# Optimization experiments

Hardware: AMD Instinct MI355X
Metric: run time of the kernel (lower is better)

Reference implementation:

```python
import jax, jax.numpy as jnp
import numpy as np

D_MODEL = 768
N_HEADS = 12
D_K = D_MODEL // N_HEADS
NEG = -1e9


def setup_inputs() -> dict:
    key = jax.random.key(0)
    ks = jax.random.split(key, 10)
    B, S = 2, 2048
    x = jax.random.normal(ks[0], (B, S, D_MODEL), dtype=jnp.float32)
    # causal mask, broadcastable over batch and heads
    mask = jnp.tril(jnp.ones((S, S), dtype=jnp.int32))[None, None]
    scale = 1.0 / np.sqrt(D_MODEL)
    def lin(k):
        return jax.random.normal(k, (D_MODEL, D_MODEL), dtype=jnp.float32) * scale
    return {
        "x": x, "mask": mask,
        "wq": lin(ks[1]), "bq": jnp.zeros((D_MODEL,), jnp.float32),
        "wk": lin(ks[2]), "bk": jnp.zeros((D_MODEL,), jnp.float32),
        "wv": lin(ks[3]), "bv": jnp.zeros((D_MODEL,), jnp.float32),
        "wo": lin(ks[4]), "bo": jnp.zeros((D_MODEL,), jnp.float32),
    }


def reference(x, mask, wq, bq, wk, bk, wv, bv, wo, bo):
    B, S, _ = x.shape
    def split_heads(t):  # [B,S,D] -> [B,H,S,dk]
        return t.reshape(B, S, N_HEADS, D_K).transpose(0, 2, 1, 3)
    q = split_heads(x @ wq + bq)
    k = split_heads(x @ wk + bk)
    v = split_heads(x @ wv + bv)
    scores = jnp.einsum("bhqd,bhkd->bhqk", q, k) / jnp.sqrt(jnp.float32(D_K))
    scores = jnp.where(mask == 0, NEG, scores)
    attn = jax.nn.softmax(scores, axis=-1)
    # dropout is identity in eval mode
    ctx = jnp.einsum("bhqk,bhkd->bhqd", attn, v)
    ctx = ctx.transpose(0, 2, 1, 3).reshape(B, S, D_MODEL)
    return ctx @ wo + bo
```

## Files before the change

kernel.cpp:

```cpp
#include <hip/hip_runtime.h>
#include <hip/hip_bf16.h>
#include <stdint.h>

#define DM   768
#define NH   12
#define DKH  64
#define BB   2
#define SS   2048
#define MT   (BB*SS)
#define NQKV (3*DM)

typedef __attribute__((ext_vector_type(8))) short short8;
typedef __attribute__((ext_vector_type(4))) float f32x4;

__device__ __forceinline__ unsigned short f2bf(float f) {
    union { float f; unsigned u; } v; v.f = f;
    unsigned r = v.u + 0x7fffu + ((v.u >> 16) & 1u);
    return (unsigned short)(r >> 16);
}

__device__ __forceinline__ void gload_lds16(const unsigned short* g, unsigned short* l) {
    __builtin_amdgcn_global_load_lds((const __attribute__((address_space(1))) void*)g,
                                     (__attribute__((address_space(3))) void*)l, 16, 0, 0);
}

__launch_bounds__(256)
__global__ void k_conv(const float* __restrict__ x, unsigned short* __restrict__ xb,
                       const float* __restrict__ wq, const float* __restrict__ wk,
                       const float* __restrict__ wv, const float* __restrict__ wo,
                       unsigned short* __restrict__ wT) {
    __shared__ float tile[32][33];
    const int t = threadIdx.x;
    if (blockIdx.x < 3072) {
        int i = blockIdx.x * 256 + t;
        const float4 v = ((const float4*)x)[i];
        ushort4 o;
        o.x = f2bf(v.x); o.y = f2bf(v.y); o.z = f2bf(v.z); o.w = f2bf(v.w);
        ((ushort4*)xb)[i] = o;
    } else {
        const int cid = blockIdx.x - 3072;
        const int sel = cid / 576;
        const int rem = cid - sel * 576;
        const int kb = rem / 24, nb = rem - (rem / 24) * 24;
        const float* w = (sel == 0) ? wq : (sel == 1) ? wk : (sel == 2) ? wv : wo;
        const int k0 = kb * 32, n0 = nb * 32;
        const int tx = t & 31, ty = t >> 5;
        #pragma unroll
        for (int j = 0; j < 4; j++)
            tile[ty + 8*j][tx] = w[(size_t)(k0 + ty + 8*j) * DM + n0 + tx];
        __syncthreads();
        #pragma unroll
        for (int j = 0; j < 4; j++)
            wT[(size_t)(sel*DM + n0 + ty + 8*j) * DM + k0 + tx] = f2bf(tile[tx][ty + 8*j]);
    }
}

__launch_bounds__(256)
__global__ void k_gemm_qkv(const unsigned short* __restrict__ xb,
                           const unsigned short* __restrict__ wT,
                           const float* __restrict__ bq, const float* __restrict__ bk,
                           const float* __restrict__ bv,
                           unsigned short* __restrict__ Qb,
                           unsigned short* __restrict__ Kb,
                           unsigned short* __restrict__ Vt) {
    __shared__ __align__(16) unsigned short As[128][32];
    __shared__ __align__(16) unsigned short Bs[128][32];
    const int t = threadIdx.x;
    const int m0 = blockIdx.x * 128;
    const int n0 = blockIdx.y * 128;
    const int wid = t >> 6, lane = t & 63, q4 = lane >> 4, l16 = lane & 15;
    const int wm = (wid >> 1) * 64, wn = (wid & 1) * 64;

    const int srow = wid * 32 + (lane >> 2);
    const int koff = (lane & 3) * 8;
    const unsigned short* AgL = xb + (size_t)(m0 + srow) * DM + koff;
    const unsigned short* AgH = AgL + (size_t)16 * DM;
    const unsigned short* BgL = wT + (size_t)(n0 + srow) * DM + koff;
    const unsigned short* BgH = BgL + (size_t)16 * DM;
    unsigned short* ldsA1 = &As[wid*32][0];
    unsigned short* ldsA2 = &As[wid*32 + 16][0];
    unsigned short* ldsB1 = &Bs[wid*32][0];
    unsigned short* ldsB2 = &Bs[wid*32 + 16][0];

    f32x4 acc[4][4];
    for (int i = 0; i < 4; i++) for (int j = 0; j < 4; j++)
        acc[i][j] = (f32x4){0.f, 0.f, 0.f, 0.f};

    for (int kt = 0; kt < DM; kt += 32) {
        gload_lds16(AgL + kt, ldsA1);
        gload_lds16(AgH + kt, ldsA2);
        gload_lds16(BgL + kt, ldsB1);
        gload_lds16(BgH + kt, ldsB2);
        __syncthreads();
        short8 af[4], bf[4];
        for (int i = 0; i < 4; i++) af[i] = *(const short8*)&As[wm + i*16 + l16][q4*8];
        for (int i = 0; i < 4; i++) bf[i] = *(const short8*)&Bs[wn + i*16 + l16][q4*8];
        for (int mi = 0; mi < 4; mi++)
            for (int ni = 0; ni < 4; ni++)
                acc[mi][ni] = __builtin_amdgcn_mfma_f32_16x16x32_bf16(af[mi], bf[ni], acc[mi][ni], 0, 0, 0);
        __syncthreads();
    }

    const int sel = n0 / DM;
    const float* bias = (sel == 0) ? bq : (sel == 1) ? bk : bv;
    for (int ni = 0; ni < 4; ni++) {
        const int col = n0 + wn + ni*16 + l16;
        const int c = col - sel * DM;
        const float bsv = bias[c];
        const int h = c >> 6, d = c & 63;
        for (int mi = 0; mi < 4; mi++) {
            for (int r = 0; r < 4; r++) {
                const int row = m0 + wm + mi*16 + q4*4 + r;
                const int b = row >> 11, s = row & 2047;
                const int bh = b * NH + h;
                float v = acc[mi][ni][r] + bsv;
                if (sel == 0) {
                    Qb[(bh*SS + s)*DKH + d] = f2bf(v * 0.125f);
                } else if (sel == 1) {
                    Kb[(bh*SS + s)*DKH + d] = f2bf(v);
                } else {
                    Vt[(bh*DKH + d)*SS + s] = f2bf(v);
                }
            }
        }
    }
}

__launch_bounds__(256)
__global__ void k_attn(const unsigned short* __restrict__ Qb,
                       const unsigned short* __restrict__ Kb,
                       const unsigned short* __restrict__ Vt,
                       unsigned short* __restrict__ ctx) {
    __shared__ __align__(16) unsigned short Ks[2][64][72];
    __shared__ __align__(16) unsigned short Vs[2][64][72];
    __shared__ __align__(16) unsigned short P[4][16][68];
    const int t = threadIdx.x;
    const int wid = t >> 6, lane = t & 63, q4 = lane >> 4, l16 = lane & 15;
    const int lin = blockIdx.x;
    const int bh = lin % (BB * NH);
    const int qblk = 31 - lin / (BB * NH);
    const int b = bh / NH, h = bh - b * NH;
    const int qw = qblk * 64 + wid * 16;

    const unsigned short* Qp = Qb + (size_t)bh * SS * DKH;
    const unsigned short* Kp = Kb + (size_t)bh * SS * DKH;
    const unsigned short* Vp = Vt + (size_t)bh * DKH * SS;

    const int sr = t >> 3;
    const int sc = (t & 7) * 8;

    short8 qf[2];
    for (int kc = 0; kc < 2; kc++)
        qf[kc] = *(const short8*)(Qp + (qw + l16)*DKH + kc*32 + q4*8);

    f32x4 accO[4];
    for (int j = 0; j < 4; j++) accO[j] = (f32x4){0.f, 0.f, 0.f, 0.f};
    float lacc[4] = {0.f, 0.f, 0.f, 0.f};

    {
        uint4 k0 = *(const uint4*)(Kp + (size_t)(sr)      * DKH + sc);
        uint4 k1 = *(const uint4*)(Kp + (size_t)(sr + 32) * DKH + sc);
        uint4 v0 = *(const uint4*)(Vp + (size_t)(sr)      * SS  + sc);
        uint4 v1 = *(const uint4*)(Vp + (size_t)(sr + 32) * SS  + sc);
        *(uint4*)&Ks[0][sr][sc]      = k0;
        *(uint4*)&Ks[0][sr + 32][sc] = k1;
        *(uint4*)&Vs[0][sr][sc]      = v0;
        *(uint4*)&Vs[0][sr + 32][sc] = v1;
    }
    __syncthreads();

    for (int kt = 0; kt <= qblk; kt++) {
        const int cb = kt & 1, nb = cb ^ 1;
        const bool hasN = (kt < qblk);
        uint4 nk0, nk1, nv0, nv1;
        if (hasN) {
            const int kn = (kt + 1) * 64;
            nk0 = *(const uint4*)(Kp + (size_t)(kn + sr)      * DKH + sc);
            nk1 = *(const uint4*)(Kp + (size_t)(kn + sr + 32) * DKH + sc);
            nv0 = *(const uint4*)(Vp + (size_t)(sr)      * SS + kn + sc);
            nv1 = *(const uint4*)(Vp + (size_t)(sr + 32) * SS + kn + sc);
        }
        short8 kf[4][2];
        #pragma unroll
        for (int ni = 0; ni < 4; ni++)
            #pragma unroll
            for (int kc = 0; kc < 2; kc++)
                kf[ni][kc] = *(const short8*)&Ks[cb][ni*16 + l16][kc*32 + q4*8];
        f32x4 S[4];
        #pragma unroll
        for (int j = 0; j < 4; j++) S[j] = (f32x4){0.f, 0.f, 0.f, 0.f};
        #pragma unroll
        for (int ni = 0; ni < 4; ni++) {
            S[ni] = __builtin_amdgcn_mfma_f32_16x16x32_bf16(qf[0], kf[ni][0], S[ni], 0, 0, 0);
            S[ni] = __builtin_amdgcn_mfma_f32_16x16x32_bf16(qf[1], kf[ni][1], S[ni], 0, 0, 0);
        }
        short8 vf[4][2];
        #pragma unroll
        for (int ndi = 0; ndi < 4; ndi++)
            #pragma unroll
            for (int kc = 0; kc < 2; kc++)
                vf[ndi][kc] = *(const short8*)&Vs[cb][ndi*16 + l16][kc*32 + q4*8];
        if (kt == qblk) {
            #pragma unroll
            for (int ni = 0; ni < 4; ni++) {
                const int pr = q4*4, pc = ni*16 + l16;
                if (ni > wid) {
                    P[wid][pr+0][pc] = 0; P[wid][pr+1][pc] = 0;
                    P[wid][pr+2][pc] = 0; P[wid][pr+3][pc] = 0;
                    continue;
                }
                float p[4];
                if (ni == wid) {
                    #pragma unroll
                    for (int r = 0; r < 4; r++) {
                        const int qrow = qw + q4*4 + r;
                        const int key = qblk*64 + ni*16 + l16;
                        p[r] = (key > qrow) ? 0.f : __expf(S[ni][r]);
                        lacc[r] += p[r];
                    }
                } else {
                    #pragma unroll
                    for (int r = 0; r < 4; r++) { p[r] = __expf(S[ni][r]); lacc[r] += p[r]; }
                }
                union { __hip_bfloat162 v; unsigned u; } u01, u23;
                u01.v = __float22bfloat162_rn(make_float2(p[0], p[1]));
                u23.v = __float22bfloat162_rn(make_float2(p[2], p[3]));
                P[wid][pr+0][pc] = (unsigned short)(u01.u & 0xffffu);
                P[wid][pr+1][pc] = (unsigned short)(u01.u >> 16);
                P[wid][pr+2][pc] = (unsigned short)(u23.u & 0xffffu);
                P[wid][pr+3][pc] = (unsigned short)(u23.u >> 16);
            }
        } else {
            #pragma unroll
            for (int ni = 0; ni < 4; ni++) {
                float p[4];
                #pragma unroll
                for (int r = 0; r < 4; r++) { p[r] = __expf(S[ni][r]); lacc[r] += p[r]; }
                union { __hip_bfloat162 v; unsigned u; } u01, u23;
                u01.v = __float22bfloat162_rn(make_float2(p[0], p[1]));
                u23.v = __float22bfloat162_rn(make_float2(p[2], p[3]));
                const int pr = q4*4, pc = ni*16 + l16;
                P[wid][pr+0][pc] = (unsigned short)(u01.u & 0xffffu);
                P[wid][pr+1][pc] = (unsigned short)(u01.u >> 16);
                P[wid][pr+2][pc] = (unsigned short)(u23.u & 0xffffu);
                P[wid][pr+3][pc] = (unsigned short)(u23.u >> 16);
            }
        }
        asm volatile("s_waitcnt lgkmcnt(0)" ::: "memory");
        short8 pf[2];
        #pragma unroll
        for (int kc = 0; kc < 2; kc++)
            pf[kc] = *(const short8*)&P[wid][l16][kc*32 + q4*8];
        #pragma unroll
        for (int ndi = 0; ndi < 4; ndi++)
            #pragma unroll
            for (int kc = 0; kc < 2; kc++)
                accO[ndi] = __builtin_amdgcn_mfma_f32_16x16x32_bf16(pf[kc], vf[ndi][kc], accO[ndi], 0, 0, 0);
        if (hasN) {
            *(uint4*)&Ks[nb][sr][sc]      = nk0;
            *(uint4*)&Ks[nb][sr + 32][sc] = nk1;
            *(uint4*)&Vs[nb][sr][sc]      = nv0;
            *(uint4*)&Vs[nb][sr + 32][sc] = nv1;
        }
        __syncthreads();
    }

    for (int r = 0; r < 4; r++) {
        float l = lacc[r];
        for (int off = 1; off < 16; off <<= 1) l += __shfl_xor(l, off);
        const float inv = 1.0f / l;
        const int s = qw + q4*4 + r;
        for (int ni = 0; ni < 4; ni++)
            ctx[((size_t)(b*SS + s))*DM + h*64 + ni*16 + l16] = f2bf(accO[ni][r] * inv);
    }
}

__launch_bounds__(256)
__global__ void k_gemm_proj(const unsigned short* __restrict__ ctx,
                            const unsigned short* __restrict__ woT,
                            const float* __restrict__ bo,
                            float* __restrict__ out) {
    __shared__ __align__(16) unsigned short As[128][32];
    __shared__ __align__(16) unsigned short Bs[64][32];
    const int t = threadIdx.x;
    const int m0 = blockIdx.x * 128;
    const int n0 = blockIdx.y * 64;
    const int wid = t >> 6, lane = t & 63, q4 = lane >> 4, l16 = lane & 15;
    const int wm = (wid >> 1) * 64, wn = (wid & 1) * 32;

    const int srowA = wid * 32 + (lane >> 2);
    const int srowB = wid * 16 + (lane >> 2);
    const int koff = (lane & 3) * 8;
    const unsigned short* AgL = ctx + (size_t)(m0 + srowA) * DM + koff;
    const unsigned short* AgH = AgL + (size_t)16 * DM;
    const unsigned short* BgL = woT + (size_t)(n0 + srowB) * DM + koff;
    unsigned short* ldsA1 = &As[wid*32][0];
    unsigned short* ldsA2 = &As[wid*32 + 16][0];
    unsigned short* ldsB1 = &Bs[wid*16][0];

    f32x4 acc[4][2];
    for (int i = 0; i < 4; i++) for (int j = 0; j < 2; j++)
        acc[i][j] = (f32x4){0.f, 0.f, 0.f, 0.f};

    for (int kt = 0; kt < DM; kt += 32) {
        gload_lds16(AgL + kt, ldsA1);
        gload_lds16(AgH + kt, ldsA2);
        gload_lds16(BgL + kt, ldsB1);
        __syncthreads();
        short8 af[4], bf[2];
        for (int i = 0; i < 4; i++) af[i] = *(const short8*)&As[wm + i*16 + l16][q4*8];
        for (int i = 0; i < 2; i++) bf[i] = *(const short8*)&Bs[wn + i*16 + l16][q4*8];
        for (int mi = 0; mi < 4; mi++)
            for (int ni = 0; ni < 2; ni++)
                acc[mi][ni] = __builtin_amdgcn_mfma_f32_16x16x32_bf16(af[mi], bf[ni], acc[mi][ni], 0, 0, 0);
        __syncthreads();
    }

    for (int ni = 0; ni < 2; ni++) {
        const int col = n0 + wn + ni*16 + l16;
        const float bsv = bo[col];
        for (int mi = 0; mi < 4; mi++) {
            for (int r = 0; r < 4; r++) {
                const int row = m0 + wm + mi*16 + q4*4 + r;
                out[(size_t)row * DM + col] = acc[mi][ni][r] + bsv;
            }
        }
    }
}

extern "C" void kernel_launch(void* const* d_in, const int* in_sizes, int n_in,
                              void* d_out, int out_size, void* d_ws, size_t ws_size,
                              hipStream_t stream) {
    const float* x  = (const float*)d_in[0];
    const float* wq = (const float*)d_in[2];
    const float* bq = (const float*)d_in[3];
    const float* wk = (const float*)d_in[4];
    const float* bk = (const float*)d_in[5];
    const float* wv = (const float*)d_in[6];
    const float* bv = (const float*)d_in[7];
    const float* wo = (const float*)d_in[8];
    const float* bo = (const float*)d_in[9];
    float* out = (float*)d_out;

    unsigned short* xb  = (unsigned short*)d_ws;
    unsigned short* wT  = xb + (size_t)MT * DM;
    unsigned short* Qb  = wT + (size_t)4 * DM * DM;
    unsigned short* Kb  = Qb + (size_t)BB * NH * SS * DKH;
    unsigned short* Vt  = Kb + (size_t)BB * NH * SS * DKH;
    unsigned short* ctx = Vt + (size_t)BB * NH * SS * DKH;

    k_conv<<<3072 + 2304, 256, 0, stream>>>(x, xb, wq, wk, wv, wo, wT);
    dim3 g1(MT / 128, NQKV / 128);
    k_gemm_qkv<<<g1, 256, 0, stream>>>(xb, wT, bq, bk, bv, Qb, Kb, Vt);
    k_attn<<<dim3(32 * BB * NH), 256, 0, stream>>>(Qb, Kb, Vt, ctx);
    dim3 g3(MT / 128, DM / 64);
    k_gemm_proj<<<g3, 256, 0, stream>>>(ctx, wT + (size_t)3 * DM * DM, bo, out);
}
```

Measured before the change: 176.2 us.

## Restructure attention kernel: 128-row query tiles, swizzled LDS, transposed MFMA, custom block order

The attention kernel now processes 128 query rows per block, 32 per wave, so each K/V tile loaded into LDS is reused by twice as many queries. It also swaps to an XOR-swizzled unpadded LDS layout and computes S^T and O^T through swapped MFMA operands, which allows packed P stores and vectorized ctx writes. A remapped block ordering balances the causal workload, waves skip fully masked tiles, and s_setprio plus a 3-blocks-per-CU launch bound are added. The grid shrinks to 384 blocks, which may reduce occupancy, and the higher register count per wave is a risk.

Measured after the change: 185.0 us. +5.0%, slower.

```diff
diff --git a/kernel.cpp b/kernel.cpp
--- a/kernel.cpp
+++ b/kernel.cpp
@@ -126,152 +126,173 @@
     }
 }
 
-__launch_bounds__(256)
+__launch_bounds__(256, 3)
 __global__ void k_attn(const unsigned short* __restrict__ Qb,
                        const unsigned short* __restrict__ Kb,
                        const unsigned short* __restrict__ Vt,
                        unsigned short* __restrict__ ctx) {
-    __shared__ __align__(16) unsigned short Ks[2][64][72];
-    __shared__ __align__(16) unsigned short Vs[2][64][72];
-    __shared__ __align__(16) unsigned short P[4][16][68];
+    __shared__ __align__(16) unsigned short Ks[2][64*64];
+    __shared__ __align__(16) unsigned short Vs[2][64*64];
+    __shared__ __align__(16) unsigned short P2[4][32*64];
     const int t = threadIdx.x;
     const int wid = t >> 6, lane = t & 63, q4 = lane >> 4, l16 = lane & 15;
+
     const int lin = blockIdx.x;
-    const int bh = lin % (BB * NH);
-    const int qblk = 31 - lin / (BB * NH);
+    int g;
+    if (lin < 128)      g = 128 + lin;
+    else if (lin < 256) g = lin - 128;
+    else                g = 639 - lin;
+    const int bh  = g % 24;
+    const int qsb = 15 - g / 24;
+    const int KT  = 2*qsb + 1;
     const int b = bh / NH, h = bh - b * NH;
-    const int qw = qblk * 64 + wid * 16;
+    const int qw = qsb*128 + wid*32;
+    const int ktw = (qw + 31) >> 6;
 
     const unsigned short* Qp = Qb + (size_t)bh * SS * DKH;
     const unsigned short* Kp = Kb + (size_t)bh * SS * DKH;
     const unsigned short* Vp = Vt + (size_t)bh * DKH * SS;
 
-    const int sr = t >> 3;
-    const int sc = (t & 7) * 8;
-
-    short8 qf[2];
-    for (int kc = 0; kc < 2; kc++)
-        qf[kc] = *(const short8*)(Qp + (qw + l16)*DKH + kc*32 + q4*8);
-
-    f32x4 accO[4];
-    for (int j = 0; j < 4; j++) accO[j] = (f32x4){0.f, 0.f, 0.f, 0.f};
-    float lacc[4] = {0.f, 0.f, 0.f, 0.f};
+    const int sr  = t >> 3;
+    const int sc8 = (t & 7) * 8;
+    const int scs = sc8 ^ ((sr & 7) * 8);
+    const int swz = (l16 & 7) * 8;
+
+    short8 qf[2][2];
+    #pragma unroll
+    for (int c = 0; c < 2; c++)
+        #pragma unroll
+        for (int kc = 0; kc < 2; kc++)
+            qf[c][kc] = *(const short8*)(Qp + (size_t)(qw + c*16 + l16)*DKH + kc*32 + q4*8);
+
+    f32x4 accO[2][4];
+    #pragma unroll
+    for (int c = 0; c < 2; c++)
+        #pragma unroll
+        for (int j = 0; j < 4; j++) accO[c][j] = (f32x4){0.f, 0.f, 0.f, 0.f};
+    float lacc[2] = {0.f, 0.f};
 
     {
-        uint4 k0 = *(const uint4*)(Kp + (size_t)(sr)      * DKH + sc);
-        uint4 k1 = *(const uint4*)(Kp + (size_t)(sr + 32) * DKH + sc);
-        uint4 v0 = *(const uint4*)(Vp + (size_t)(sr)      * SS  + sc);
-        uint4 v1 = *(const uint4*)(Vp + (size_t)(sr + 32) * SS  + sc);
-        *(uint4*)&Ks[0][sr][sc]      = k0;
-        *(uint4*)&Ks[0][sr + 32][sc] = k1;
-        *(uint4*)&Vs[0][sr][sc]      = v0;
-        *(uint4*)&Vs[0][sr + 32][sc] = v1;
+        *(uint4*)&Ks[0][ sr      *64 + scs] = *(const uint4*)(Kp + (size_t) sr      *DKH + sc8);
+        *(uint4*)&Ks[0][(sr+32)*64 + scs]   = *(const uint4*)(Kp + (size_t)(sr+32)  *DKH + sc8);
+        *(uint4*)&Vs[0][ sr      *64 + scs] = *(const uint4*)(Vp + (size_t) sr      *SS  + sc8);
+        *(uint4*)&Vs[0][(sr+32)*64 + scs]   = *(const uint4*)(Vp + (size_t)(sr+32)  *SS  + sc8);
     }
     __syncthreads();
 
-    for (int kt = 0; kt <= qblk; kt++) {
+    for (int kt = 0; kt <= KT; kt++) {
         const int cb = kt & 1, nb = cb ^ 1;
-        const bool hasN = (kt < qblk);
+        const bool hasN = (kt < KT);
         uint4 nk0, nk1, nv0, nv1;
         if (hasN) {
             const int kn = (kt + 1) * 64;
-            nk0 = *(const uint4*)(Kp + (size_t)(kn + sr)      * DKH + sc);
-            nk1 = *(const uint4*)(Kp + (size_t)(kn + sr + 32) * DKH + sc);
-            nv0 = *(const uint4*)(Vp + (size_t)(sr)      * SS + kn + sc);
-            nv1 = *(const uint4*)(Vp + (size_t)(sr + 32) * SS + kn + sc);
-        }
-        short8 kf[4][2];
-        #pragma unroll
-        for (int ni = 0; ni < 4; ni++)
+            nk0 = *(const uint4*)(Kp + (size_t)(kn + sr)      * DKH + sc8);
+            nk1 = *(const uint4*)(Kp + (size_t)(kn + sr + 32) * DKH + sc8);
+            nv0 = *(const uint4*)(Vp + (size_t)(sr)      * SS + kn + sc8);
+            nv1 = *(const uint4*)(Vp + (size_t)(sr + 32) * SS + kn + sc8);
+        }
+        if (kt <= ktw) {
+            f32x4 St[2][4];
             #pragma unroll
-            for (int kc = 0; kc < 2; kc++)
-                kf[ni][kc] = *(const short8*)&Ks[cb][ni*16 + l16][kc*32 + q4*8];
-        f32x4 S[4];
-        #pragma unroll
-        for (int j = 0; j < 4; j++) S[j] = (f32x4){0.f, 0.f, 0.f, 0.f};
-        #pragma unroll
-        for (int ni = 0; ni < 4; ni++) {
-            S[ni] = __builtin_amdgcn_mfma_f32_16x16x32_bf16(qf[0], kf[ni][0], S[ni], 0, 0, 0);
-            S[ni] = __builtin_amdgcn_mfma_f32_16x16x32_bf16(qf[1], kf[ni][1], S[ni], 0, 0, 0);
-        }
-        short8 vf[4][2];
-        #pragma unroll
-        for (int ndi = 0; ndi < 4; ndi++)
-            #pragma unroll
-            for (int kc = 0; kc < 2; kc++)
-                vf[ndi][kc] = *(const short8*)&Vs[cb][ndi*16 + l16][kc*32 + q4*8];
-        if (kt == qblk) {
+            for (int c = 0; c < 2; c++)
+                #pragma unroll
+                for (int ni = 0; ni < 4; ni++) St[c][ni] = (f32x4){0.f, 0.f, 0.f, 0.f};
+            __builtin_amdgcn_s_setprio(1);
             #pragma unroll
             for (int ni = 0; ni < 4; ni++) {
-                const int pr = q4*4, pc = ni*16 + l16;
-                if (ni > wid) {
-                    P[wid][pr+0][pc] = 0; P[wid][pr+1][pc] = 0;
-                    P[wid][pr+2][pc] = 0; P[wid][pr+3][pc] = 0;
-                    continue;
+                const int rbase = (ni*16 + l16) * 64;
+                short8 kf0 = *(const short8*)&Ks[cb][rbase + ((     q4*8) ^ swz)];
+                short8 kf1 = *(const short8*)&Ks[cb][rbase + ((32 + q4*8) ^ swz)];
+                St[0][ni] = __builtin_amdgcn_mfma_f32_16x16x32_bf16(kf0, qf[0][0], St[0][ni], 0, 0, 0);
+                St[0][ni] = __builtin_amdgcn_mfma_f32_16x16x32_bf16(kf1, qf[0][1], St[0][ni], 0, 0, 0);
+                St[1][ni] = __builtin_amdgcn_mfma_f32_16x16x32_bf16(kf0, qf[1][0], St[1][ni], 0, 0, 0);
+                St[1][ni] = __builtin_amdgcn_mfma_f32_16x16x32_bf16(kf1, qf[1][1], St[1][ni], 0, 0, 0);
+            }
+            __builtin_amdgcn_s_setprio(0);
+            if (kt < ktw) {
+                #pragma unroll
+                for (int c = 0; c < 2; c++) {
+                    const int prow = (c*16 + l16) * 64;
+                    #pragma unroll
+                    for (int ni = 0; ni < 4; ni++) {
+                        float p0 = __expf(St[c][ni][0]), p1 = __expf(St[c][ni][1]);
+                        float p2 = __expf(St[c][ni][2]), p3 = __expf(St[c][ni][3]);
+                        lacc[c] += (p0 + p1) + (p2 + p3);
+                        union { __hip_bfloat162 v; unsigned u; } u01, u23;
+                        u01.v = __float22bfloat162_rn(make_float2(p0, p1));
+                        u23.v = __float22bfloat162_rn(make_float2(p2, p3));
+                        uint2 pk; pk.x = u01.u; pk.y = u23.u;
+                        *(uint2*)&P2[wid][prow + ((ni*16 + q4*4) ^ swz)] = pk;
+                    }
                 }
-                float p[4];
-                if (ni == wid) {
+            } else {
+                const int kb0 = kt * 64;
+                #pragma unroll
+                for (int c = 0; c < 2; c++) {
+                    const int qrow = qw + c*16 + l16;
+                    const int prow = (c*16 + l16) * 64;
                     #pragma unroll
-                    for (int r = 0; r < 4; r++) {
-                        const int qrow = qw + q4*4 + r;
-                        const int key = qblk*64 + ni*16 + l16;
-                        p[r] = (key > qrow) ? 0.f : __expf(S[ni][r]);
-                        lacc[r] += p[r];
+                    for (int ni = 0; ni < 4; ni++) {
+                        const int key0 = kb0 + ni*16 + q4*4;
+                        float p[4];
+                        #pragma unroll
+                        for (int r = 0; r < 4; r++) {
+                            p[r] = (key0 + r > qrow) ? 0.f : __expf(St[c][ni][r]);
+                            lacc[c] += p[r];
+                        }
+                        union { __hip_bfloat162 v; unsigned u; } u01, u23;
+                        u01.v = __float22bfloat162_rn(make_float2(p[0], p[1]));
+                        u23.v = __float22bfloat162_rn(make_float2(p[2], p[3]));
+                        uint2 pk; pk.x = u01.u; pk.y = u23.u;
+                        *(uint2*)&P2[wid][prow + ((ni*16 + q4*4) ^ swz)] = pk;
                     }
-                } else {
-                    #pragma unroll
-                    for (int r = 0; r < 4; r++) { p[r] = __expf(S[ni][r]); lacc[r] += p[r]; }
                 }
-                union { __hip_bfloat162 v; unsigned u; } u01, u23;
-                u01.v = __float22bfloat162_rn(make_float2(p[0], p[1]));
-                u23.v = __float22bfloat162_rn(make_float2(p[2], p[3]));
-                P[wid][pr+0][pc] = (unsigned short)(u01.u & 0xffffu);
-                P[wid][pr+1][pc] = (unsigned short)(u01.u >> 16);
-                P[wid][pr+2][pc] = (unsigned short)(u23.u & 0xffffu);
-                P[wid][pr+3][pc] = (unsigned short)(u23.u >> 16);
-            }
-        } else {
+            }
+            asm volatile("s_waitcnt lgkmcnt(0)" ::: "memory");
+            short8 pf[2][2];
             #pragma unroll
-            for (int ni = 0; ni < 4; ni++) {
-                float p[4];
+            for (int c = 0; c < 2; c++)
                 #pragma unroll
-                for (int r = 0; r < 4; r++) { p[r] = __expf(S[ni][r]); lacc[r] += p[r]; }
-                union { __hip_bfloat162 v; unsigned u; } u01, u23;
-                u01.v = __float22bfloat162_rn(make_float2(p[0], p[1]));
-                u23.v = __float22bfloat162_rn(make_float2(p[2], p[3]));
-                const int pr = q4*4, pc = ni*16 + l16;
-                P[wid][pr+0][pc] = (unsigned short)(u01.u & 0xffffu);
-                P[wid][pr+1][pc] = (unsigned short)(u01.u >> 16);
-                P[wid][pr+2][pc] = (unsigned short)(u23.u & 0xffffu);
-                P[wid][pr+3][pc] = (unsigned short)(u23.u >> 16);
-            }
-        }
-        asm volatile("s_waitcnt lgkmcnt(0)" ::: "memory");
-        short8 pf[2];
-        #pragma unroll
-        for (int kc = 0; kc < 2; kc++)
-            pf[kc] = *(const short8*)&P[wid][l16][kc*32 + q4*8];
-        #pragma unroll
-        for (int ndi = 0; ndi < 4; ndi++)
+                for (int kc = 0; kc < 2; kc++)
+                    pf[c][kc] = *(const short8*)&P2[wid][(c*16 + l16)*64 + ((kc*32 + q4*8) ^ swz)];
+            __builtin_amdgcn_s_setprio(1);
             #pragma unroll
-            for (int kc = 0; kc < 2; kc++)
-                accO[ndi] = __builtin_amdgcn_mfma_f32_16x16x32_bf16(pf[kc], vf[ndi][kc], accO[ndi], 0, 0, 0);
+            for (int ndi = 0; ndi < 4; ndi++) {
+                const int rbase = (ndi*16 + l16) * 64;
+                short8 vf0 = *(const short8*)&Vs[cb][rbase + ((     q4*8) ^ swz)];
+                short8 vf1 = *(const short8*)&Vs[cb][rbase + ((32 + q4*8) ^ swz)];
+                accO[0][ndi] = __builtin_amdgcn_mfma_f32_16x16x32_bf16(vf0, pf[0][0], accO[0][ndi], 0, 0, 0);
+                accO[0][ndi] = __builtin_amdgcn_mfma_f32_16x16x32_bf16(vf1, pf[0][1], accO[0][ndi], 0, 0, 0);
+                accO[1][ndi] = __builtin_amdgcn_mfma_f32_16x16x32_bf16(vf0, pf[1][0], accO[1][ndi], 0, 0, 0);
+                accO[1][ndi] = __builtin_amdgcn_mfma_f32_16x16x32_bf16(vf1, pf[1][1], accO[1][ndi], 0, 0, 0);
+            }
+            __builtin_amdgcn_s_setprio(0);
+        }
         if (hasN) {
-            *(uint4*)&Ks[nb][sr][sc]      = nk0;
-            *(uint4*)&Ks[nb][sr + 32][sc] = nk1;
-            *(uint4*)&Vs[nb][sr][sc]      = nv0;
-            *(uint4*)&Vs[nb][sr + 32][sc] = nv1;
-        }
-        __syncthreads();
-    }
-
-    for (int r = 0; r < 4; r++) {
-        float l = lacc[r];
-        for (int off = 1; off < 16; off <<= 1) l += __shfl_xor(l, off);
+            *(uint4*)&Ks[nb][ sr     *64 + scs] = nk0;
+            *(uint4*)&Ks[nb][(sr+32)*64 + scs]  = nk1;
+            *(uint4*)&Vs[nb][ sr     *64 + scs] = nv0;
+            *(uint4*)&Vs[nb][(sr+32)*64 + scs]  = nv1;
+        }
+        __syncthreads();
+    }
+
+    #pragma unroll
+    for (int c = 0; c < 2; c++) {
+        float l = lacc[c];
+        l += __shfl_xor(l, 16);
+        l += __shfl_xor(l, 32);
         const float inv = 1.0f / l;
-        const int s = qw + q4*4 + r;
-        for (int ni = 0; ni < 4; ni++)
-            ctx[((size_t)(b*SS + s))*DM + h*64 + ni*16 + l16] = f2bf(accO[ni][r] * inv);
+        const size_t row = (size_t)(b*SS + qw + c*16 + l16);
+        #pragma unroll
+        for (int ndi = 0; ndi < 4; ndi++) {
+            ushort4 o;
+            o.x = f2bf(accO[c][ndi][0] * inv);
+            o.y = f2bf(accO[c][ndi][1] * inv);
+            o.z = f2bf(accO[c][ndi][2] * inv);
+            o.w = f2bf(accO[c][ndi][3] * inv);
+            *(ushort4*)&ctx[row*DM + h*64 + ndi*16 + q4*4] = o;
+        }
     }
 }
 
@@ -352,7 +373,7 @@
     k_conv<<<3072 + 2304, 256, 0, stream>>>(x, xb, wq, wk, wv, wo, wT);
     dim3 g1(MT / 128, NQKV / 128);
     k_gemm_qkv<<<g1, 256, 0, stream>>>(xb, wT, bq, bk, bv, Qb, Kb, Vt);
-    k_attn<<<dim3(32 * BB * NH), 256, 0, stream>>>(Qb, Kb, Vt, ctx);
+    k_attn<<<dim3(384), 256, 0, stream>>>(Qb, Kb, Vt, ctx);
     dim3 g3(MT / 128, DM / 64);
     k_gemm_proj<<<g3, 256, 0, stream>>>(ctx, wT + (size_t)3 * DM * DM, bo, out);
 }
```
